# Performance work log

Measured on AMD Instinct MI355X. Metric: run time of the kernel, lower is better.

The kernel has to match this reference:

```python
import jax, jax.numpy as jnp
import numpy as np

T, B, E, H, L, V = 35, 128, 200, 512, 2, 10000


def setup_inputs() -> dict:
    key = jax.random.key(0)
    ks = jax.random.split(key, 8)
    s = 0.05  # weight init scale
    return {
        "inputs": jax.random.randint(ks[0], (T, B), 0, V),
        "hidden": jnp.zeros((L, B, H), jnp.float32),
        "emb": jax.random.normal(ks[1], (V, E), jnp.float32) * s,
        "Wx0": jax.random.normal(ks[2], (3, H, E), jnp.float32) * s,
        "Wx": jax.random.normal(ks[3], (L - 1, 3, H, H), jnp.float32) * s,
        "Wh": jax.random.normal(ks[4], (L, 3, H, H), jnp.float32) * s,
        "bh": jax.random.normal(ks[5], (L, 3, H), jnp.float32) * s,
        "Wout": jax.random.normal(ks[6], (V, H), jnp.float32) * s,
        "bout": jnp.zeros((V,), jnp.float32),
    }


def reference(inputs, hidden, emb, Wx0, Wx, Wh, bh, Wout, bout):
    # inputs: [T,B] int; hidden: [L,B,H]
    x = emb[inputs]  # [T,B,E]
    num_layers = hidden.shape[0]

    def step(h_prev, x_t):
        data = x_t  # dropout is identity (keep_prob=1.0)
        new_h = []
        for j in range(num_layers):
            Wxj = Wx0 if j == 0 else Wx[j - 1]
            gx = jnp.einsum('bi,ghi->gbh', data, Wxj)  # [3,B,H], no bias on x-side
            hp = h_prev[j]
            reset = jax.nn.sigmoid(gx[0] + hp @ Wh[j, 0].T + bh[j, 0])
            forget = jax.nn.sigmoid(gx[1] + hp @ Wh[j, 1].T + bh[j, 1])
            tild = jnp.tanh(gx[2] + (reset * hp) @ Wh[j, 2].T + bh[j, 2])
            hn = (1.0 - forget) * hp + forget * tild
            new_h.append(hn)
            data = hn  # dropout identity
        logit = data @ Wout.T + bout  # [B,V]
        return jnp.stack(new_h), logit

    h_final, logits = jax.lax.scan(step, hidden, x)
    return logits, h_final
```

## Files before the change

### kernel.cpp

```cpp
#include <hip/hip_runtime.h>
#include <hip/hip_bf16.h>

#define T_ 35
#define B_ 128
#define E_ 200
#define H_ 512
#define L_ 2
#define V_ 10000
#define BH_ (B_ * H_)
#define KPAD 224
#define NCL 4
#define CLW 48
#define NWG (NCL * CLW)

typedef __attribute__((ext_vector_type(8))) short bf16x8;
typedef __attribute__((ext_vector_type(4))) float f32x4;

__device__ __forceinline__ unsigned short f2bf(float f) {
    union { float f; unsigned u; } c; c.f = f;
    unsigned r = c.u + 0x7FFF + ((c.u >> 16) & 1);
    return (unsigned short)(r >> 16);
}
__device__ __forceinline__ float bf2f(unsigned short u) {
    union { unsigned u; float f; } c; c.u = ((unsigned)u) << 16; return c.f;
}

__device__ __forceinline__ bf16x8 cvt8(const float* src) {
    float4 w0 = *(const float4*)src;
    float4 w1 = *(const float4*)(src + 4);
    bf16x8 v;
    v[0] = (short)f2bf(w0.x); v[1] = (short)f2bf(w0.y);
    v[2] = (short)f2bf(w0.z); v[3] = (short)f2bf(w0.w);
    v[4] = (short)f2bf(w1.x); v[5] = (short)f2bf(w1.y);
    v[6] = (short)f2bf(w1.z); v[7] = (short)f2bf(w1.w);
    return v;
}

__device__ __forceinline__ void store_quad_bf16(unsigned short* buf, int idx,
                                                float v, int lane) {
    unsigned x = (unsigned)f2bf(v);
    unsigned y = (unsigned)__shfl_xor((int)x, 1);
    unsigned pair = (lane & 1) ? (y | (x << 16)) : (x | (y << 16));
    unsigned long long q = (unsigned long long)pair;
    unsigned long long p2 = (unsigned long long)(unsigned)__shfl_xor((int)pair, 2);
    unsigned long long quad = (lane & 2) ? (p2 | (q << 32)) : (q | (p2 << 32));
    if ((lane & 3) == 0)
        __hip_atomic_store((unsigned long long*)(buf + idx), quad,
                           __ATOMIC_RELAXED, __HIP_MEMORY_SCOPE_AGENT);
}

__global__ void prep_all(const float* __restrict__ emb, const float* __restrict__ Wx0,
                         const float* __restrict__ hidden, const float* __restrict__ Wout,
                         unsigned short* embB, unsigned short* wx0cat,
                         unsigned short* WoutB,
                         unsigned short* h0bt, unsigned short* h1bfx, int* flags) {
    int job = blockIdx.y;
    int stride = gridDim.x * blockDim.x;
    int i0 = blockIdx.x * blockDim.x + threadIdx.x;
    if (job == 0) {
        for (int i = i0; i < V_ * KPAD; i += stride) {
            int v = i / KPAD, k = i - v * KPAD;
            embB[i] = (k < E_) ? f2bf(emb[v * E_ + k]) : (unsigned short)0;
        }
    } else if (job == 1) {
        for (int i = i0; i < 1536 * KPAD; i += stride) {
            int n = i / KPAD, k = i - n * KPAD;
            wx0cat[i] = (k < E_) ? f2bf(Wx0[n * E_ + k]) : (unsigned short)0;
        }
    } else if (job == 2) {
        for (int i = i0; i < 2 * BH_; i += stride) {
            if (i < BH_) h0bt[i] = f2bf(hidden[i]);
            else         h1bfx[i - BH_] = f2bf(hidden[i]);
        }
        for (int i = i0; i < NWG * 32; i += stride) flags[i] = 0;
    } else {
        for (int i = i0; i < V_ * H_; i += stride) WoutB[i] = f2bf(Wout[i]);
    }
}

__global__ __launch_bounds__(256) void xside_gemm(
    const int* __restrict__ inputs, const unsigned short* __restrict__ embB,
    const unsigned short* __restrict__ wx0cat, float* __restrict__ gx0) {
    int m0 = blockIdx.x * 128, n0 = blockIdx.y * 128;
    int wave = threadIdx.x >> 6, lane = threadIdx.x & 63;
    int wr = wave >> 1, wc = wave & 1;
    int am = m0 + wr * 64, bn = n0 + wc * 64;
    int lr = lane & 15, lk = (lane >> 4) * 8;

    f32x4 acc[4][4] = {};
    int id[4];
    #pragma unroll
    for (int i = 0; i < 4; ++i) id[i] = inputs[am + i * 16 + lr];

    for (int k0 = 0; k0 < KPAD; k0 += 32) {
        bf16x8 a[4], b[4];
        #pragma unroll
        for (int i = 0; i < 4; ++i)
            a[i] = *(const bf16x8*)(embB + (size_t)id[i] * KPAD + k0 + lk);
        #pragma unroll
        for (int j = 0; j < 4; ++j)
            b[j] = *(const bf16x8*)(wx0cat + (size_t)(bn + j * 16 + lr) * KPAD + k0 + lk);
        #pragma unroll
        for (int i = 0; i < 4; ++i)
            #pragma unroll
            for (int j = 0; j < 4; ++j)
                acc[i][j] = __builtin_amdgcn_mfma_f32_16x16x32_bf16(a[i], b[j], acc[i][j], 0, 0, 0);
    }
    int crow0 = (lane >> 4) * 4, ccol = lane & 15;
    #pragma unroll
    for (int i = 0; i < 4; ++i) {
        #pragma unroll
        for (int r = 0; r < 4; ++r) {
            int row = am + i * 16 + crow0 + r;
            int t = row >> 7, b = row & 127;
            #pragma unroll
            for (int j = 0; j < 4; ++j) {
                int col = bn + j * 16 + ccol;
                int g = col >> 9, h = col & 511;
                gx0[((size_t)(t * 3 + g) * 128 + b) * 512 + h] = acc[i][j][r];
            }
        }
    }
}

__device__ __forceinline__ void bar_l0(int* flb, int wgl, int gen) {
    __syncthreads();
    if (threadIdx.x == 0)
        __hip_atomic_store(flb + wgl * 32, gen,
                           __ATOMIC_RELAXED, __HIP_MEMORY_SCOPE_AGENT);
    if (threadIdx.x < 16) {
        while (__hip_atomic_load(flb + threadIdx.x * 32, __ATOMIC_RELAXED,
                                 __HIP_MEMORY_SCOPE_AGENT) < gen)
            __builtin_amdgcn_s_sleep(1);
    }
    __syncthreads();
}

__device__ __forceinline__ void bar_l1(int* flb, int wid, int gen, int l0need) {
    __syncthreads();
    if (threadIdx.x == 0)
        __hip_atomic_store(flb + (16 + wid) * 32, gen,
                           __ATOMIC_RELAXED, __HIP_MEMORY_SCOPE_AGENT);
    if (threadIdx.x < 32) {
        while (__hip_atomic_load(flb + (16 + threadIdx.x) * 32, __ATOMIC_RELAXED,
                                 __HIP_MEMORY_SCOPE_AGENT) < gen)
            __builtin_amdgcn_s_sleep(1);
    } else if (threadIdx.x < 48) {
        while (__hip_atomic_load(flb + (threadIdx.x - 32) * 32, __ATOMIC_RELAXED,
                                 __HIP_MEMORY_SCOPE_AGENT) < l0need)
            __builtin_amdgcn_s_sleep(1);
    }
    __syncthreads();
}

__global__ __launch_bounds__(512) void scan_kernel(
    const float* __restrict__ gx0,
    const float* __restrict__ Wx, const float* __restrict__ Wh,
    const float* __restrict__ bh, const float* __restrict__ hidden,
    unsigned short* h0bt, unsigned short* rh0t, unsigned short* rh1t,
    unsigned short* h1bfx, int* flags, float* hfinal_out) {
    __shared__ unsigned short wlds[96 * 512];

    const int tid = threadIdx.x;
    const int bx = blockIdx.x;
    const int cl = bx & 3;
    const int wgl = bx >> 2;
    const int lane = tid & 63;
    const int wave = tid >> 6;
    const int lr = lane & 15;
    const int hi = lane >> 4;
    const int lk8 = hi * 8;
    const int ccol = lane & 15;
    const int crow0 = hi * 4;
    const int R0 = cl * 32;

    const bool isL0 = (wgl < 16);
    const int wid = wgl - 16;
    int* flb = flags + cl * CLW * 32;

    if (isL0) {
        for (int i = tid; i < 96 * 64; i += 512) {
            int lc = i >> 6, kg = i & 63;
            int g = lc >> 5, h = (wgl << 5) + (lc & 31);
            const float* src = Wh + (size_t)(g * 512 + h) * 512 + kg * 8;
            *(bf16x8*)(wlds + lc * 512 + (kg ^ (lc & 7)) * 8) = cvt8(src);
        }
    } else {
        for (int i = tid; i < 48 * 128; i += 512) {
            int lc = i >> 7, kg = i & 127;
            int g = lc >> 4, h = (wid << 4) + (lc & 15);
            const float* src = (kg < 64)
                ? Wx + (size_t)(g * 512 + h) * 512 + kg * 8
                : Wh + (size_t)(3 * 512 * 512) + (size_t)(g * 512 + h) * 512 + (kg - 64) * 8;
            *(bf16x8*)(wlds + lc * 1024 + (kg ^ (lc & 7)) * 8) = cvt8(src);
        }
    }

    const int mt0 = wave >> 2, nt0 = wave & 3;
    const int mt1 = (wave >> 1) & 1, nt1 = wave & 1;
    float h0reg[4], freg0[4], bias_p1_0 = 0.f, bias_p2_0 = 0.f;
    float h1reg[4], freg1[4], bias_p1_1 = 0.f, bias_p2_1 = 0.f;
    bf16x8 a0keep[16];

    if (isL0) {
        const int base = wgl << 5;
        int g = nt0 >> 1;
        int hp1 = base + (nt0 & 1) * 16 + ccol;
        bias_p1_0 = bh[g * 512 + hp1];
        if (nt0 >= 2) {
            int hc = base + (nt0 - 2) * 16 + ccol;
            int rowg = R0 + mt0 * 16;
            #pragma unroll
            for (int r = 0; r < 4; ++r)
                h0reg[r] = hidden[(size_t)(rowg + crow0 + r) * 512 + hc];
            bias_p2_0 = bh[1024 + hc];
        }
    } else {
        const int base = wid << 4;
        int hc = base + ccol;
        if (wave < 4) {
            bias_p1_1 = bh[1536 + nt1 * 512 + hc];
            if (nt1 == 1) {
                int rowg = R0 + mt1 * 16;
                #pragma unroll
                for (int r = 0; r < 4; ++r)
                    h1reg[r] = hidden[(size_t)BH_ + (size_t)(rowg + crow0 + r) * 512 + hc];
                bias_p2_1 = bh[2560 + hc];
            }
        }
    }
    __syncthreads();

    if (isL0) {
        const int base = wgl << 5;
        const int rowg = R0 + mt0 * 16;
        const int hP1 = base + (nt0 & 1) * 16 + ccol;
        const int gP1 = nt0 >> 1;
        const int ntp = (nt0 >= 2) ? (nt0 - 2) : 0;
        const int hP2 = base + ntp * 16 + ccol;

        float gxn[4];
        {
            const float* gx = gx0 + (size_t)(0 * 3 + gP1) * BH_ + hP1;
            #pragma unroll
            for (int r = 0; r < 4; ++r)
                gxn[r] = gx[(rowg + crow0 + r) * 512];
        }

        for (int s = 0; s < 2 * T_; ++s) {
            bar_l0(flb, wgl, s);
            int t = s >> 1;
            float gxc[4];
            #pragma unroll
            for (int r = 0; r < 4; ++r) gxc[r] = gxn[r];
            if (s + 1 < 2 * T_) {
                int tn = (s + 1) >> 1;
                const float* gx = (((s + 1) & 1) == 0)
                    ? gx0 + (size_t)(tn * 3 + gP1) * BH_ + hP1
                    : gx0 + (size_t)(tn * 3 + 2) * BH_ + hP2;
                #pragma unroll
                for (int r = 0; r < 4; ++r)
                    gxn[r] = gx[(rowg + crow0 + r) * 512];
            }
            if ((s & 1) == 0) {
                const unsigned short* hprev = h0bt + (size_t)t * BH_;
                unsigned short* rh0 = rh0t + (size_t)t * BH_;
                bf16x8 a[16];
                #pragma unroll
                for (int ks = 0; ks < 16; ++ks)
                    a[ks] = *(const bf16x8*)(hprev + (size_t)(rowg + lr) * 512 + ks * 32 + lk8);
                f32x4 accA = {0.f, 0.f, 0.f, 0.f}, accB = {0.f, 0.f, 0.f, 0.f};
                #pragma unroll
                for (int ks = 0; ks < 16; ks += 2) {
                    int c = nt0 * 16 + lr;
                    int kgA = 4 * ks + hi, kgB = 4 * (ks + 1) + hi;
                    bf16x8 bA = *(const bf16x8*)(wlds + c * 512 + (kgA ^ (c & 7)) * 8);
                    bf16x8 bB = *(const bf16x8*)(wlds + c * 512 + (kgB ^ (c & 7)) * 8);
                    accA = __builtin_amdgcn_mfma_f32_16x16x32_bf16(a[ks], bA, accA, 0, 0, 0);
                    accB = __builtin_amdgcn_mfma_f32_16x16x32_bf16(a[ks + 1], bB, accB, 0, 0, 0);
                }
                #pragma unroll
                for (int r = 0; r < 4; ++r) {
                    int b = rowg + crow0 + r;
                    float v = accA[r] + accB[r] + gxc[r] + bias_p1_0;
                    float sg = 1.f / (1.f + __expf(-v));
                    if (nt0 < 2) {
                        float h0p = bf2f(hprev[(size_t)b * 512 + hP1]);
                        store_quad_bf16(rh0, b * 512 + hP1 - (lane & 3), sg * h0p, lane);
                    } else {
                        freg0[r] = sg;
                    }
                }
            } else if (nt0 >= 2) {
                const unsigned short* rh0 = rh0t + (size_t)t * BH_;
                unsigned short* h0nx = h0bt + (size_t)(t + 1) * BH_;
                bf16x8 a[16];
                #pragma unroll
                for (int ks = 0; ks < 16; ++ks)
                    a[ks] = *(const bf16x8*)(rh0 + (size_t)(rowg + lr) * 512 + ks * 32 + lk8);
                f32x4 accA = {0.f, 0.f, 0.f, 0.f}, accB = {0.f, 0.f, 0.f, 0.f};
                #pragma unroll
                for (int ks = 0; ks < 16; ks += 2) {
                    int c = 64 + ntp * 16 + lr;
                    int kgA = 4 * ks + hi, kgB = 4 * (ks + 1) + hi;
                    bf16x8 bA = *(const bf16x8*)(wlds + c * 512 + (kgA ^ (c & 7)) * 8);
                    bf16x8 bB = *(const bf16x8*)(wlds + c * 512 + (kgB ^ (c & 7)) * 8);
                    accA = __builtin_amdgcn_mfma_f32_16x16x32_bf16(a[ks], bA, accA, 0, 0, 0);
                    accB = __builtin_amdgcn_mfma_f32_16x16x32_bf16(a[ks + 1], bB, accB, 0, 0, 0);
                }
                #pragma unroll
                for (int r = 0; r < 4; ++r) {
                    int b = rowg + crow0 + r;
                    float v = accA[r] + accB[r] + gxc[r] + bias_p2_0;
                    float tld = tanhf(v);
                    float hn = h0reg[r] + freg0[r] * (tld - h0reg[r]);
                    h0reg[r] = hn;
                    store_quad_bf16(h0nx, b * 512 + hP2 - (lane & 3), hn, lane);
                }
            }
        }
        __syncthreads();
        if (tid == 0)
            __hip_atomic_store(flb + wgl * 32, 2 * T_,
                               __ATOMIC_RELAXED, __HIP_MEMORY_SCOPE_AGENT);
        if (nt0 >= 2) {
            #pragma unroll
            for (int r = 0; r < 4; ++r)
                hfinal_out[(size_t)(rowg + crow0 + r) * 512 + hP2] = h0reg[r];
        }
    } else {
        for (int s = 0; s < 2 * T_; ++s) {
            int tc = s >> 1;
            int l0need = ((s & 1) == 0) ? (2 * tc + 2) : 0;
            bar_l1(flb, wid, s, l0need);
            if ((s & 1) == 0) {
                if (wave < 4) {
                    const int base = wid << 4;
                    const int rowg = R0 + mt1 * 16;
                    const unsigned short* h0cur = h0bt + (size_t)(tc + 1) * BH_;
                    const unsigned short* h1prev = h1bfx + (size_t)tc * BH_;
                    unsigned short* rh1 = rh1t + (size_t)tc * BH_;
                    bf16x8 a1[16];
                    #pragma unroll
                    for (int ks = 0; ks < 16; ++ks) {
                        a0keep[ks] = *(const bf16x8*)(h0cur + (size_t)(rowg + lr) * 512 + ks * 32 + lk8);
                        a1[ks] = *(const bf16x8*)(h1prev + (size_t)(rowg + lr) * 512 + ks * 32 + lk8);
                    }
                    f32x4 accA = {0.f, 0.f, 0.f, 0.f}, accB = {0.f, 0.f, 0.f, 0.f};
                    #pragma unroll
                    for (int ks = 0; ks < 16; ++ks) {
                        int kg = 4 * ks + hi;
                        int c = nt1 * 16 + lr;
                        bf16x8 b = *(const bf16x8*)(wlds + c * 1024 + (kg ^ (c & 7)) * 8);
                        accA = __builtin_amdgcn_mfma_f32_16x16x32_bf16(a0keep[ks], b, accA, 0, 0, 0);
                    }
                    #pragma unroll
                    for (int ks = 0; ks < 16; ++ks) {
                        int kg = 64 + 4 * ks + hi;
                        int c = nt1 * 16 + lr;
                        bf16x8 b = *(const bf16x8*)(wlds + c * 1024 + (kg ^ (c & 7)) * 8);
                        accB = __builtin_amdgcn_mfma_f32_16x16x32_bf16(a1[ks], b, accB, 0, 0, 0);
                    }
                    int h = base + ccol;
                    #pragma unroll
                    for (int r = 0; r < 4; ++r) {
                        int b = rowg + crow0 + r;
                        float v = accA[r] + accB[r] + bias_p1_1;
                        float sg = 1.f / (1.f + __expf(-v));
                        if (nt1 == 0) {
                            float h1p = bf2f(h1prev[(size_t)b * 512 + h]);
                            store_quad_bf16(rh1, b * 512 + h - (lane & 3), sg * h1p, lane);
                        } else {
                            freg1[r] = sg;
                        }
                    }
                }
            } else {
                if (wave < 4 && nt1 == 1) {
                    const int base = wid << 4;
                    const int rowg = R0 + mt1 * 16;
                    const unsigned short* rh1 = rh1t + (size_t)tc * BH_;
                    unsigned short* h1nx = h1bfx + (size_t)(tc + 1) * BH_;
                    bf16x8 a1[16];
                    #pragma unroll
                    for (int ks = 0; ks < 16; ++ks)
                        a1[ks] = *(const bf16x8*)(rh1 + (size_t)(rowg + lr) * 512 + ks * 32 + lk8);
                    f32x4 accA = {0.f, 0.f, 0.f, 0.f}, accB = {0.f, 0.f, 0.f, 0.f};
                    #pragma unroll
                    for (int ks = 0; ks < 16; ++ks) {
                        int kg = 4 * ks + hi;
                        int c = 32 + lr;
                        bf16x8 b = *(const bf16x8*)(wlds + c * 1024 + (kg ^ (c & 7)) * 8);
                        accA = __builtin_amdgcn_mfma_f32_16x16x32_bf16(a0keep[ks], b, accA, 0, 0, 0);
                    }
                    #pragma unroll
                    for (int ks = 0; ks < 16; ++ks) {
                        int kg = 64 + 4 * ks + hi;
                        int c = 32 + lr;
                        bf16x8 b = *(const bf16x8*)(wlds + c * 1024 + (kg ^ (c & 7)) * 8);
                        accB = __builtin_amdgcn_mfma_f32_16x16x32_bf16(a1[ks], b, accB, 0, 0, 0);
                    }
                    int h = base + ccol;
                    #pragma unroll
                    for (int r = 0; r < 4; ++r) {
                        int b = rowg + crow0 + r;
                        float v = accA[r] + accB[r] + bias_p2_1;
                        float tld = tanhf(v);
                        float hn = h1reg[r] + freg1[r] * (tld - h1reg[r]);
                        h1reg[r] = hn;
                        store_quad_bf16(h1nx, b * 512 + h - (lane & 3), hn, lane);
                    }
                }
            }
        }
        if (wave < 4 && nt1 == 1) {
            const int base = wid << 4;
            int rowg = R0 + mt1 * 16;
            #pragma unroll
            for (int r = 0; r < 4; ++r)
                hfinal_out[(size_t)BH_ + (size_t)(rowg + crow0 + r) * 512 + base + ccol] = h1reg[r];
        }
    }
}

#define MT_ (T_ * B_ / 128)
#define NT_ ((V_ + 127) / 128)
__global__ __launch_bounds__(256) void logits_gemm(
    const unsigned short* __restrict__ A, const unsigned short* __restrict__ Bw,
    const float* __restrict__ bout, float* __restrict__ C) {
    const int nwg = MT_ * NT_;
    const int q = nwg / 8, rr = nwg % 8;
    int bid = blockIdx.x;
    int xcd = bid % 8, idx = bid / 8;
    int wgid = (xcd < rr ? xcd * (q + 1) : rr * (q + 1) + (xcd - rr) * q) + idx;
    int n0 = (wgid / MT_) * 128;
    int m0 = (wgid % MT_) * 128;

    int wave = threadIdx.x >> 6, lane = threadIdx.x & 63;
    int wr = wave >> 1, wc = wave & 1;
    int am = m0 + wr * 64, bn = n0 + wc * 64;
    int lr = lane & 15, lk = (lane >> 4) * 8;

    f32x4 acc[4][4] = {};
    bf16x8 a[4], b[4], an[4], bnx[4];
    #pragma unroll
    for (int i = 0; i < 4; ++i)
        a[i] = *(const bf16x8*)(A + (size_t)(am + i * 16 + lr) * H_ + lk);
    #pragma unroll
    for (int j = 0; j < 4; ++j) {
        int colc = bn + j * 16 + lr; if (colc >= V_) colc = V_ - 1;
        b[j] = *(const bf16x8*)(Bw + (size_t)colc * H_ + lk);
    }
    for (int k0 = 0; k0 < H_; k0 += 32) {
        if (k0 + 32 < H_) {
            #pragma unroll
            for (int i = 0; i < 4; ++i)
                an[i] = *(const bf16x8*)(A + (size_t)(am + i * 16 + lr) * H_ + k0 + 32 + lk);
            #pragma unroll
            for (int j = 0; j < 4; ++j) {
                int colc = bn + j * 16 + lr; if (colc >= V_) colc = V_ - 1;
                bnx[j] = *(const bf16x8*)(Bw + (size_t)colc * H_ + k0 + 32 + lk);
            }
        }
        #pragma unroll
        for (int i = 0; i < 4; ++i)
            #pragma unroll
            for (int j = 0; j < 4; ++j)
                acc[i][j] = __builtin_amdgcn_mfma_f32_16x16x32_bf16(a[i], b[j], acc[i][j], 0, 0, 0);
        #pragma unroll
        for (int i = 0; i < 4; ++i) { a[i] = an[i]; b[i] = bnx[i]; }
    }
    int crow0 = (lane >> 4) * 4, ccol = lane & 15;
    #pragma unroll
    for (int j = 0; j < 4; ++j) {
        int col = bn + j * 16 + ccol;
        if (col >= V_) continue;
        float bv = bout[col];
        #pragma unroll
        for (int i = 0; i < 4; ++i) {
            #pragma unroll
            for (int r = 0; r < 4; ++r) {
                int row = am + i * 16 + crow0 + r;
                __builtin_nontemporal_store(acc[i][j][r] + bv, &C[(size_t)row * V_ + col]);
            }
        }
    }
}

extern "C" void kernel_launch(void* const* d_in, const int* in_sizes, int n_in,
                              void* d_out, int out_size, void* d_ws, size_t ws_size,
                              hipStream_t stream) {
    const int*   inputs = (const int*)  d_in[0];
    const float* hidden = (const float*)d_in[1];
    const float* emb    = (const float*)d_in[2];
    const float* Wx0    = (const float*)d_in[3];
    const float* Wx     = (const float*)d_in[4];
    const float* Wh     = (const float*)d_in[5];
    const float* bh     = (const float*)d_in[6];
    const float* Wout   = (const float*)d_in[7];
    const float* bout   = (const float*)d_in[8];
    float* out = (float*)d_out;
    (void)in_sizes; (void)n_in; (void)out_size; (void)ws_size;

    char* ws = (char*)d_ws;
    size_t off = 0;
    auto alloc = [&](size_t bytes) -> void* {
        void* p = ws + off;
        off += (bytes + 255) & ~(size_t)255;
        return p;
    };
    unsigned short* embB   = (unsigned short*)alloc((size_t)V_ * KPAD * 2);
    unsigned short* wx0cat = (unsigned short*)alloc((size_t)1536 * KPAD * 2);
    unsigned short* WoutB  = (unsigned short*)alloc((size_t)V_ * H_ * 2);
    unsigned short* h1bfx  = (unsigned short*)alloc((size_t)(T_ + 1) * BH_ * 2);
    int* flags = (int*)alloc(NWG * 32 * 4);

    float* gx0 = out;
    unsigned short* scr = (unsigned short*)(out + (size_t)T_ * 3 * BH_);
    unsigned short* h0bt = scr;
    unsigned short* rh0t = scr + (size_t)(T_ + 1) * BH_;
    unsigned short* rh1t = scr + (size_t)(2 * T_ + 1) * BH_;

    prep_all<<<dim3(1024, 4), dim3(256), 0, stream>>>(
        emb, Wx0, hidden, Wout, embB, wx0cat, WoutB, h0bt, h1bfx, flags);
    xside_gemm<<<dim3(T_, 12), dim3(256), 0, stream>>>(inputs, embB, wx0cat, gx0);
    scan_kernel<<<dim3(NWG), dim3(512), 0, stream>>>(
        gx0, Wx, Wh, bh, hidden,
        h0bt, rh0t, rh1t, h1bfx, flags,
        out + (size_t)T_ * B_ * V_);
    logits_gemm<<<dim3(MT_ * NT_), dim3(256), 0, stream>>>(
        h1bfx + BH_, WoutB, bout, out);
}
```

Measured before the change: 595.1 us.

## Fuse emb/Wx0 bf16 conversion into x-side GEMM and enlarge logits tiles

Drops the full-vocabulary embedding and Wx0 bf16 conversion passes from the prep kernel. xside_gemm now reads fp32 emb and Wx0 directly and converts them in registers with a validity mask for the K padding, so only the gathered rows get touched. Separately, the logits GEMM moves from 128x128 tiles with 4 waves to 256x256 tiles with 8 waves, with row clamping and guarded stores for the partial last M tile. The larger tiles raise operand reuse but increase register pressure and leave fewer workgroups (720), with wasted work at the M and N edges.

```diff
diff --git a/kernel.cpp b/kernel.cpp
--- a/kernel.cpp
+++ b/kernel.cpp
@@ -49,25 +49,13 @@
                            __ATOMIC_RELAXED, __HIP_MEMORY_SCOPE_AGENT);
 }
 
-__global__ void prep_all(const float* __restrict__ emb, const float* __restrict__ Wx0,
-                         const float* __restrict__ hidden, const float* __restrict__ Wout,
-                         unsigned short* embB, unsigned short* wx0cat,
+__global__ void prep_all(const float* __restrict__ hidden, const float* __restrict__ Wout,
                          unsigned short* WoutB,
                          unsigned short* h0bt, unsigned short* h1bfx, int* flags) {
     int job = blockIdx.y;
     int stride = gridDim.x * blockDim.x;
     int i0 = blockIdx.x * blockDim.x + threadIdx.x;
     if (job == 0) {
-        for (int i = i0; i < V_ * KPAD; i += stride) {
-            int v = i / KPAD, k = i - v * KPAD;
-            embB[i] = (k < E_) ? f2bf(emb[v * E_ + k]) : (unsigned short)0;
-        }
-    } else if (job == 1) {
-        for (int i = i0; i < 1536 * KPAD; i += stride) {
-            int n = i / KPAD, k = i - n * KPAD;
-            wx0cat[i] = (k < E_) ? f2bf(Wx0[n * E_ + k]) : (unsigned short)0;
-        }
-    } else if (job == 2) {
         for (int i = i0; i < 2 * BH_; i += stride) {
             if (i < BH_) h0bt[i] = f2bf(hidden[i]);
             else         h1bfx[i - BH_] = f2bf(hidden[i]);
@@ -79,8 +67,8 @@
 }
 
 __global__ __launch_bounds__(256) void xside_gemm(
-    const int* __restrict__ inputs, const unsigned short* __restrict__ embB,
-    const unsigned short* __restrict__ wx0cat, float* __restrict__ gx0) {
+    const int* __restrict__ inputs, const float* __restrict__ emb,
+    const float* __restrict__ Wx0, float* __restrict__ gx0) {
     int m0 = blockIdx.x * 128, n0 = blockIdx.y * 128;
     int wave = threadIdx.x >> 6, lane = threadIdx.x & 63;
     int wr = wave >> 1, wc = wave & 1;
@@ -92,14 +80,17 @@
     #pragma unroll
     for (int i = 0; i < 4; ++i) id[i] = inputs[am + i * 16 + lr];
 
+    bf16x8 zb = {0,0,0,0,0,0,0,0};
     for (int k0 = 0; k0 < KPAD; k0 += 32) {
+        int kg = k0 + lk;
+        bool valid = (kg < E_);
         bf16x8 a[4], b[4];
         #pragma unroll
         for (int i = 0; i < 4; ++i)
-            a[i] = *(const bf16x8*)(embB + (size_t)id[i] * KPAD + k0 + lk);
+            a[i] = valid ? cvt8(emb + (size_t)id[i] * E_ + kg) : zb;
         #pragma unroll
         for (int j = 0; j < 4; ++j)
-            b[j] = *(const bf16x8*)(wx0cat + (size_t)(bn + j * 16 + lr) * KPAD + k0 + lk);
+            b[j] = valid ? cvt8(Wx0 + (size_t)(bn + j * 16 + lr) * E_ + kg) : zb;
         #pragma unroll
         for (int i = 0; i < 4; ++i)
             #pragma unroll
@@ -423,52 +414,58 @@
     }
 }
 
-#define MT_ (T_ * B_ / 128)
-#define NT_ ((V_ + 127) / 128)
-__global__ __launch_bounds__(256) void logits_gemm(
+#define MT2 18
+#define NT2 40
+__global__ __launch_bounds__(512) void logits_gemm(
     const unsigned short* __restrict__ A, const unsigned short* __restrict__ Bw,
     const float* __restrict__ bout, float* __restrict__ C) {
-    const int nwg = MT_ * NT_;
-    const int q = nwg / 8, rr = nwg % 8;
+    const int nwg = MT2 * NT2;
+    const int q = nwg / 8;
     int bid = blockIdx.x;
-    int xcd = bid % 8, idx = bid / 8;
-    int wgid = (xcd < rr ? xcd * (q + 1) : rr * (q + 1) + (xcd - rr) * q) + idx;
-    int n0 = (wgid / MT_) * 128;
-    int m0 = (wgid % MT_) * 128;
+    int wgid = (bid % 8) * q + bid / 8;
+    int n0 = (wgid / MT2) * 256;
+    int m0 = (wgid % MT2) * 256;
 
     int wave = threadIdx.x >> 6, lane = threadIdx.x & 63;
-    int wr = wave >> 1, wc = wave & 1;
-    int am = m0 + wr * 64, bn = n0 + wc * 64;
+    int wr = wave >> 2;
+    int wc = wave & 3;
+    int am = m0 + wr * 128, bn = n0 + wc * 64;
     int lr = lane & 15, lk = (lane >> 4) * 8;
 
-    f32x4 acc[4][4] = {};
-    bf16x8 a[4], b[4], an[4], bnx[4];
+    f32x4 acc[8][4] = {};
+    bf16x8 a[8], b[4], an[8], bnx[4];
     #pragma unroll
-    for (int i = 0; i < 4; ++i)
-        a[i] = *(const bf16x8*)(A + (size_t)(am + i * 16 + lr) * H_ + lk);
+    for (int i = 0; i < 8; ++i) {
+        int row = am + i * 16 + lr; if (row >= T_ * B_) row = T_ * B_ - 1;
+        a[i] = *(const bf16x8*)(A + (size_t)row * H_ + lk);
+    }
     #pragma unroll
     for (int j = 0; j < 4; ++j) {
-        int colc = bn + j * 16 + lr; if (colc >= V_) colc = V_ - 1;
-        b[j] = *(const bf16x8*)(Bw + (size_t)colc * H_ + lk);
+        int col = bn + j * 16 + lr; if (col >= V_) col = V_ - 1;
+        b[j] = *(const bf16x8*)(Bw + (size_t)col * H_ + lk);
     }
     for (int k0 = 0; k0 < H_; k0 += 32) {
         if (k0 + 32 < H_) {
             #pragma unroll
-            for (int i = 0; i < 4; ++i)
-                an[i] = *(const bf16x8*)(A + (size_t)(am + i * 16 + lr) * H_ + k0 + 32 + lk);
+            for (int i = 0; i < 8; ++i) {
+                int row = am + i * 16 + lr; if (row >= T_ * B_) row = T_ * B_ - 1;
+                an[i] = *(const bf16x8*)(A + (size_t)row * H_ + k0 + 32 + lk);
+            }
             #pragma unroll
             for (int j = 0; j < 4; ++j) {
-                int colc = bn + j * 16 + lr; if (colc >= V_) colc = V_ - 1;
-                bnx[j] = *(const bf16x8*)(Bw + (size_t)colc * H_ + k0 + 32 + lk);
-            }
-        }
-        #pragma unroll
-        for (int i = 0; i < 4; ++i)
+                int col = bn + j * 16 + lr; if (col >= V_) col = V_ - 1;
+                bnx[j] = *(const bf16x8*)(Bw + (size_t)col * H_ + k0 + 32 + lk);
+            }
+        }
+        #pragma unroll
+        for (int i = 0; i < 8; ++i)
             #pragma unroll
             for (int j = 0; j < 4; ++j)
                 acc[i][j] = __builtin_amdgcn_mfma_f32_16x16x32_bf16(a[i], b[j], acc[i][j], 0, 0, 0);
         #pragma unroll
-        for (int i = 0; i < 4; ++i) { a[i] = an[i]; b[i] = bnx[i]; }
+        for (int i = 0; i < 8; ++i) a[i] = an[i];
+        #pragma unroll
+        for (int j = 0; j < 4; ++j) b[j] = bnx[j];
     }
     int crow0 = (lane >> 4) * 4, ccol = lane & 15;
     #pragma unroll
@@ -477,11 +474,12 @@
         if (col >= V_) continue;
         float bv = bout[col];
         #pragma unroll
-        for (int i = 0; i < 4; ++i) {
+        for (int i = 0; i < 8; ++i) {
             #pragma unroll
             for (int r = 0; r < 4; ++r) {
                 int row = am + i * 16 + crow0 + r;
-                __builtin_nontemporal_store(acc[i][j][r] + bv, &C[(size_t)row * V_ + col]);
+                if (row < T_ * B_)
+                    __builtin_nontemporal_store(acc[i][j][r] + bv, &C[(size_t)row * V_ + col]);
             }
         }
     }
@@ -509,10 +507,8 @@
         off += (bytes + 255) & ~(size_t)255;
         return p;
     };
-    unsigned short* embB   = (unsigned short*)alloc((size_t)V_ * KPAD * 2);
-    unsigned short* wx0cat = (unsigned short*)alloc((size_t)1536 * KPAD * 2);
-    unsigned short* WoutB  = (unsigned short*)alloc((size_t)V_ * H_ * 2);
-    unsigned short* h1bfx  = (unsigned short*)alloc((size_t)(T_ + 1) * BH_ * 2);
+    unsigned short* WoutB = (unsigned short*)alloc((size_t)V_ * H_ * 2);
+    unsigned short* h1bfx = (unsigned short*)alloc((size_t)(T_ + 1) * BH_ * 2);
     int* flags = (int*)alloc(NWG * 32 * 4);
 
     float* gx0 = out;
@@ -521,13 +517,13 @@
     unsigned short* rh0t = scr + (size_t)(T_ + 1) * BH_;
     unsigned short* rh1t = scr + (size_t)(2 * T_ + 1) * BH_;
 
-    prep_all<<<dim3(1024, 4), dim3(256), 0, stream>>>(
-        emb, Wx0, hidden, Wout, embB, wx0cat, WoutB, h0bt, h1bfx, flags);
-    xside_gemm<<<dim3(T_, 12), dim3(256), 0, stream>>>(inputs, embB, wx0cat, gx0);
+    prep_all<<<dim3(1024, 2), dim3(256), 0, stream>>>(
+        hidden, Wout, WoutB, h0bt, h1bfx, flags);
+    xside_gemm<<<dim3(T_, 12), dim3(256), 0, stream>>>(inputs, emb, Wx0, gx0);
     scan_kernel<<<dim3(NWG), dim3(512), 0, stream>>>(
         gx0, Wx, Wh, bh, hidden,
         h0bt, rh0t, rh1t, h1bfx, flags,
         out + (size_t)T_ * B_ * V_);
-    logits_gemm<<<dim3(MT_ * NT_), dim3(256), 0, stream>>>(
+    logits_gemm<<<dim3(MT2 * NT2), dim3(512), 0, stream>>>(
         h1bfx + BH_, WoutB, bout, out);
 }
```

Measured after the change: 619.0 us. +4.0%, slower.
